# Performance work log

Measured on AMD Instinct MI355X. Metric: run time of the kernel, lower is better.

Reference implementation:

```python
import jax, jax.numpy as jnp
import numpy as np

B, N, C, H = 8, 1024, 768, 12
D = C // H  # head dim
SCALE = D ** -0.5


def setup_inputs() -> dict:
    key = jax.random.key(0)
    ks = jax.random.split(key, 5)
    return {
        "x": jax.random.normal(ks[0], (B, N, C), dtype=jnp.float32),
        "W_qkv": jax.random.normal(ks[1], (C, 3 * C), dtype=jnp.float32) * (C ** -0.5),
        "b_qkv": jax.random.normal(ks[2], (3 * C,), dtype=jnp.float32) * 0.02,
        "W_proj": jax.random.normal(ks[3], (C, C), dtype=jnp.float32) * (C ** -0.5),
        "b_proj": jax.random.normal(ks[4], (C,), dtype=jnp.float32) * 0.02,
    }


def reference(x, W_qkv, b_qkv, W_proj, b_proj):
    b, n, c = x.shape
    qkv = x @ W_qkv + b_qkv                      # [B,N,3C]
    # rearrange 'b n (k h c) -> k b h n c'
    qkv = qkv.reshape(b, n, 3, H, D).transpose(2, 0, 3, 1, 4)
    q, k, v = qkv[0] * SCALE, qkv[1], qkv[2]     # each [B,H,N,D]
    p = jax.nn.softmax(jnp.einsum('bhnd,bhmd->bhnm', q, k), axis=-1)
    o = jnp.einsum('bhnm,bhmd->bhnd', p, v)      # [B,H,N,D]
    o = o.transpose(0, 2, 1, 3).reshape(b, n, c)  # 'b h n c -> b n (h c)'
    return o @ W_proj + b_proj
```

## Files before the change

kernel.cpp:

```cpp
#include <hip/hip_runtime.h>


typedef short  bf16x8_t __attribute__((ext_vector_type(8)));
typedef float  f32x4_t  __attribute__((ext_vector_type(4)));

static __device__ __forceinline__ unsigned short f2bf(float f) {
    union { float f; unsigned u; } v; v.f = f;
    unsigned r = v.u + 0x7fffu + ((v.u >> 16) & 1u);
    return (unsigned short)(r >> 16);
}

typedef __attribute__((address_space(1))) const unsigned gas_u32;
typedef __attribute__((address_space(3))) unsigned las_u32;
static __device__ __forceinline__ void gload16(const void* g, void* l) {
    __builtin_amdgcn_global_load_lds((gas_u32*)g, (las_u32*)l, 16, 0, 0);
}

#define WAIT0 asm volatile("s_waitcnt vmcnt(0)" ::: "memory")
#define BAR   __builtin_amdgcn_s_barrier()

#define STAGE_TILE(DST, SRC, K0, NP, NT)                                   \
    _Pragma("unroll")                                                      \
    for (int p_ = 0; p_ < NP; ++p_) {                                      \
        const int base_ = p_*NT + wb;                                      \
        const int i_ = base_ + lane;                                       \
        const int row_ = i_ >> 3;                                          \
        const int cb_ = ((i_ & 7) ^ (row_ & 7)) * 8;                       \
        gload16((SRC) + (size_t)row_*768 + (K0) + cb_, &(DST)[base_*8]);   \
    }

#define COMPUTE_T(AS, BS)                                                  \
    {                                                                      \
        bf16x8_t a_[2][4], b_[2][4];                                       \
        _Pragma("unroll")                                                  \
        for (int ks_ = 0; ks_ < 2; ++ks_) {                                \
            _Pragma("unroll")                                              \
            for (int m_ = 0; m_ < 4; ++m_) {                               \
                const int ra_ = wm*64 + m_*16 + l15;                       \
                a_[ks_][m_] = *(const bf16x8_t*)&(AS)[ra_*64 + ((ks_*4 + lhi) ^ (ra_ & 7))*8]; \
                const int rb_ = wn*64 + m_*16 + l15;                       \
                b_[ks_][m_] = *(const bf16x8_t*)&(BS)[rb_*64 + ((ks_*4 + lhi) ^ (rb_ & 7))*8]; \
            }                                                              \
        }                                                                  \
        _Pragma("unroll")                                                  \
        for (int m_ = 0; m_ < 4; ++m_)                                     \
            _Pragma("unroll")                                              \
            for (int n_ = 0; n_ < 4; ++n_) {                               \
                acc[m_][n_] = __builtin_amdgcn_mfma_f32_16x16x32_bf16(a_[0][m_], b_[0][n_], acc[m_][n_], 0, 0, 0); \
                acc[m_][n_] = __builtin_amdgcn_mfma_f32_16x16x32_bf16(a_[1][m_], b_[1][n_], acc[m_][n_], 0, 0, 0); \
            }                                                              \
    }

#define COMPUTE_P(AS, BS)                                                  \
    {                                                                      \
        bf16x8_t a_[2][2], b_[2][4];                                       \
        _Pragma("unroll")                                                  \
        for (int ks_ = 0; ks_ < 2; ++ks_) {                                \
            _Pragma("unroll")                                              \
            for (int m_ = 0; m_ < 2; ++m_) {                               \
                const int ra_ = wm*32 + m_*16 + l15;                       \
                a_[ks_][m_] = *(const bf16x8_t*)&(AS)[ra_*64 + ((ks_*4 + lhi) ^ (ra_ & 7))*8]; \
            }                                                              \
            _Pragma("unroll")                                              \
            for (int n_ = 0; n_ < 4; ++n_) {                               \
                const int rb_ = wn*64 + n_*16 + l15;                       \
                b_[ks_][n_] = *(const bf16x8_t*)&(BS)[rb_*64 + ((ks_*4 + lhi) ^ (rb_ & 7))*8]; \
            }                                                              \
        }                                                                  \
        _Pragma("unroll")                                                  \
        for (int m_ = 0; m_ < 2; ++m_)                                     \
            _Pragma("unroll")                                              \
            for (int n_ = 0; n_ < 4; ++n_) {                               \
                acc[m_][n_] = __builtin_amdgcn_mfma_f32_16x16x32_bf16(a_[0][m_], b_[0][n_], acc[m_][n_], 0, 0, 0); \
                acc[m_][n_] = __builtin_amdgcn_mfma_f32_16x16x32_bf16(a_[1][m_], b_[1][n_], acc[m_][n_], 0, 0, 0); \
            }                                                              \
    }

__global__ __launch_bounds__(256) void convert_x(
    const float* __restrict__ src, unsigned short* __restrict__ dst)
{
    const int i = blockIdx.x * 256 + threadIdx.x;
    const float4 v = ((const float4*)src)[i];
    ushort4 o; o.x = f2bf(v.x); o.y = f2bf(v.y); o.z = f2bf(v.z); o.w = f2bf(v.w);
    ((ushort4*)dst)[i] = o;
}

__global__ __launch_bounds__(256) void transpose_cvt(
    const float* __restrict__ src, unsigned short* __restrict__ dst, int R, int C)
{
    __shared__ unsigned short tile[32][33];
    const int tx = threadIdx.x & 31, ty = threadIdx.x >> 5;
    const int bx = blockIdx.x, by = blockIdx.y;
    #pragma unroll
    for (int j = 0; j < 32; j += 8)
        tile[ty + j][tx] = f2bf(src[(size_t)(by*32 + ty + j) * C + bx*32 + tx]);
    __syncthreads();
    #pragma unroll
    for (int j = 0; j < 32; j += 8)
        dst[(size_t)(bx*32 + ty + j) * R + by*32 + tx] = tile[tx][ty + j];
}

__global__ __launch_bounds__(512, 4) void gemm_qkv_bf16(
    const unsigned short* __restrict__ A, const unsigned short* __restrict__ Bt,
    const float* __restrict__ bias,
    unsigned short* __restrict__ q, unsigned short* __restrict__ kO,
    unsigned short* __restrict__ vT)
{
    __shared__ unsigned short As[256*64];
    __shared__ unsigned short Bs[128*64];
    const int tid = threadIdx.x;
    const int id = blockIdx.x;
    const int swz = (id & 7) * 72 + (id >> 3);
    const int n0 = (swz % 18) * 128, m0 = (swz / 18) * 256;

    const int lane = tid & 63, w = tid >> 6;
    const int l15 = lane & 15, lhi = lane >> 4;
    const int wm = w >> 1, wn = w & 1;
    const int wb = tid & 448;

    const unsigned short* Ab = A  + (size_t)m0 * 768;
    const unsigned short* Bb = Bt + (size_t)n0 * 768;

    f32x4_t acc[4][4] = {};

    #pragma unroll 1
    for (int t = 0; t < 12; ++t) {
        STAGE_TILE(As, Ab, t*64, 4, 512)
        STAGE_TILE(Bs, Bb, t*64, 2, 512)
        WAIT0; BAR;
        COMPUTE_T(As, Bs)
        BAR;
    }

    #pragma unroll
    for (int n = 0; n < 4; ++n) {
        const int gcol = n0 + wn*64 + n*16 + l15;
        const int kk = gcol / 768;
        const int r  = gcol - kk*768;
        const int h  = r >> 6, d = r & 63;
        const float bv = bias[gcol];
        const float sc = (kk == 0) ? 0.125f : 1.0f;
        #pragma unroll
        for (int m = 0; m < 4; ++m) {
            const int grow_base = m0 + wm*64 + m*16 + lhi*4;
            #pragma unroll
            for (int reg = 0; reg < 4; ++reg) {
                const int grow = grow_base + reg;
                const int bb = grow >> 10, seq = grow & 1023;
                const unsigned short ov = f2bf((acc[m][n][reg] + bv) * sc);
                const size_t bh = (size_t)bb*12 + h;
                if (kk == 0)      q [ (bh*1024 + seq)*64 + d ] = ov;
                else if (kk == 1) kO[ (bh*1024 + seq)*64 + d ] = ov;
                else              vT[ (bh*64 + d)*1024 + seq ] = ov;
            }
        }
    }
}

__global__ __launch_bounds__(256, 5) void attn2(
    const unsigned short* __restrict__ q, const unsigned short* __restrict__ k,
    const unsigned short* __restrict__ vT, unsigned short* __restrict__ obuf)
{
    __shared__ unsigned short Ks[64 * 72];
    __shared__ unsigned short Vs[64 * 72];
    __shared__ unsigned short P[4][16 * 72];
    const int tid = threadIdx.x;
    const int id = blockIdx.x;
    const int swz = (id & 7) * 192 + (id >> 3);
    const int qt = swz & 15, bh = swz >> 4;

    const int lane = tid & 63, w = tid >> 6;
    const int l15 = lane & 15, lhi = lane >> 4;
    const unsigned short* qp = q  + (size_t)bh * 65536;
    const unsigned short* kp = k  + (size_t)bh * 65536;
    const unsigned short* vp = vT + (size_t)bh * 65536;

    bf16x8_t qf[2];
    const int qrow = qt*64 + w*16 + l15;
    #pragma unroll
    for (int ks = 0; ks < 2; ++ks)
        qf[ks] = *(const bf16x8_t*)(qp + (size_t)qrow*64 + ks*32 + lhi*8);

    f32x4_t acco[4] = {};
    float lsum[4] = {0.f, 0.f, 0.f, 0.f};
    unsigned short* Pw = P[w];

    const int rr = (tid & 127) >> 1 | ((tid >> 7) << 6);
    (void)rr;

    bf16x8_t kr[2], vr[2];
    #pragma unroll
    for (int p = 0; p < 2; ++p) {
        const int idx = p*256 + tid;
        const int r8 = idx >> 3, cb = (idx & 7) * 8;
        kr[p] = *(const bf16x8_t*)(kp + (size_t)r8*64 + cb);
        vr[p] = *(const bf16x8_t*)(vp + (size_t)r8*1024 + cb);
    }
    #pragma unroll
    for (int p = 0; p < 2; ++p) {
        const int idx = p*256 + tid;
        const int r8 = idx >> 3, cb = (idx & 7) * 8;
        *(bf16x8_t*)&Ks[r8*72 + cb] = kr[p];
        *(bf16x8_t*)&Vs[r8*72 + cb] = vr[p];
    }

    for (int kt = 0; kt < 16; ++kt) {
        __syncthreads();
        if (kt < 15) {
            #pragma unroll
            for (int p = 0; p < 2; ++p) {
                const int idx = p*256 + tid;
                const int r8 = idx >> 3, cb = (idx & 7) * 8;
                kr[p] = *(const bf16x8_t*)(kp + (size_t)((kt+1)*64 + r8)*64 + cb);
                vr[p] = *(const bf16x8_t*)(vp + (size_t)r8*1024 + (kt+1)*64 + cb);
            }
        }

        f32x4_t accs[4] = {};
        __builtin_amdgcn_s_setprio(1);
        #pragma unroll
        for (int c = 0; c < 4; ++c)
            #pragma unroll
            for (int ks = 0; ks < 2; ++ks) {
                bf16x8_t kf = *(const bf16x8_t*)&Ks[(c*16 + l15)*72 + ks*32 + lhi*8];
                accs[c] = __builtin_amdgcn_mfma_f32_16x16x32_bf16(qf[ks], kf, accs[c], 0, 0, 0);
            }
        __builtin_amdgcn_s_setprio(0);

        #pragma unroll
        for (int c = 0; c < 4; ++c)
            #pragma unroll
            for (int r = 0; r < 4; ++r) {
                const float pv = __expf(accs[c][r]);
                lsum[r] += pv;
                Pw[(lhi*4 + r)*72 + c*16 + l15] = f2bf(pv);
            }

        bf16x8_t pf[2];
        #pragma unroll
        for (int ks = 0; ks < 2; ++ks)
            pf[ks] = *(const bf16x8_t*)&Pw[l15*72 + ks*32 + lhi*8];
        __builtin_amdgcn_s_setprio(1);
        #pragma unroll
        for (int n = 0; n < 4; ++n)
            #pragma unroll
            for (int ks = 0; ks < 2; ++ks) {
                bf16x8_t vf = *(const bf16x8_t*)&Vs[(n*16 + l15)*72 + ks*32 + lhi*8];
                acco[n] = __builtin_amdgcn_mfma_f32_16x16x32_bf16(pf[ks], vf, acco[n], 0, 0, 0);
            }
        __builtin_amdgcn_s_setprio(0);

        __syncthreads();
        if (kt < 15) {
            #pragma unroll
            for (int p = 0; p < 2; ++p) {
                const int idx = p*256 + tid;
                const int r8 = idx >> 3, cb = (idx & 7) * 8;
                *(bf16x8_t*)&Ks[r8*72 + cb] = kr[p];
                *(bf16x8_t*)&Vs[r8*72 + cb] = vr[p];
            }
        }
    }

    #pragma unroll
    for (int r = 0; r < 4; ++r)
        #pragma unroll
        for (int off = 1; off <= 8; off <<= 1)
            lsum[r] += __shfl_xor(lsum[r], off, 64);

    const int b = bh / 12, h = bh % 12;
    #pragma unroll
    for (int n = 0; n < 4; ++n)
        #pragma unroll
        for (int r = 0; r < 4; ++r) {
            const int seq = qt*64 + w*16 + lhi*4 + r;
            obuf[((size_t)(b*1024 + seq))*768 + h*64 + n*16 + l15] = f2bf(acco[n][r] / lsum[r]);
        }
}

__global__ __launch_bounds__(256, 4) void gemm_proj_bf16(
    const unsigned short* __restrict__ A, const unsigned short* __restrict__ Bt,
    const float* __restrict__ bias, float* __restrict__ out)
{
    __shared__ unsigned short As[64*64];
    __shared__ unsigned short Bs[128*64];
    const int tid = threadIdx.x;
    const int id = blockIdx.x;
    const int swz = (id & 7) * 96 + (id >> 3);
    const int n0 = (swz % 6) * 128, m0 = (swz / 6) * 64;

    const int lane = tid & 63, w = tid >> 6;
    const int l15 = lane & 15, lhi = lane >> 4;
    const int wm = w >> 1, wn = w & 1;
    const int wb = tid & 192;

    const unsigned short* Ab = A  + (size_t)m0 * 768;
    const unsigned short* Bb = Bt + (size_t)n0 * 768;

    f32x4_t acc[2][4] = {};

    #pragma unroll 1
    for (int t = 0; t < 12; ++t) {
        STAGE_TILE(As, Ab, t*64, 2, 256)
        STAGE_TILE(Bs, Bb, t*64, 4, 256)
        WAIT0; BAR;
        COMPUTE_P(As, Bs)
        BAR;
    }

    #pragma unroll
    for (int n = 0; n < 4; ++n) {
        const int gcol = n0 + wn*64 + n*16 + l15;
        const float bv = bias[gcol];
        #pragma unroll
        for (int m = 0; m < 2; ++m) {
            const int grow_base = m0 + wm*32 + m*16 + lhi*4;
            #pragma unroll
            for (int reg = 0; reg < 4; ++reg)
                out[(size_t)(grow_base + reg)*768 + gcol] = acc[m][n][reg] + bv;
        }
    }
}

extern "C" void kernel_launch(void* const* d_in, const int* in_sizes, int n_in,
                              void* d_out, int out_size, void* d_ws, size_t ws_size,
                              hipStream_t stream) {
    const float* x     = (const float*)d_in[0];
    const float* Wqkv  = (const float*)d_in[1];
    const float* bqkv  = (const float*)d_in[2];
    const float* Wproj = (const float*)d_in[3];
    const float* bproj = (const float*)d_in[4];
    float* out = (float*)d_out;
    unsigned short* ws = (unsigned short*)d_ws;

    unsigned short* xb    = ws;
    unsigned short* obuf  = ws;
    unsigned short* wqt   = ws + 6291456u;
    unsigned short* wpt   = ws + 8060928u;
    unsigned short* qb    = ws + 8650752u;
    unsigned short* kb    = ws + 14942208u;
    unsigned short* vTb   = ws + 21233664u;

    convert_x     <<<6144, 256, 0, stream>>>(x, xb);
    transpose_cvt <<<dim3(72, 24), 256, 0, stream>>>(Wqkv, wqt, 768, 2304);
    transpose_cvt <<<dim3(24, 24), 256, 0, stream>>>(Wproj, wpt, 768, 768);
    gemm_qkv_bf16 <<<576, 512, 0, stream>>>(xb, wqt, bqkv, qb, kb, vTb);
    attn2         <<<1536, 256, 0, stream>>>(qb, kb, vTb, obuf);
    gemm_proj_bf16<<<768, 256, 0, stream>>>(obuf, wpt, bproj, out);
}
```

Measured before the change: 136.8 us.

## Restructure QKV GEMM into 256x256 double-buffered tiles with interleaved prefetch

```diff
diff --git a/kernel.cpp b/kernel.cpp
--- a/kernel.cpp
+++ b/kernel.cpp
@@ -18,6 +18,45 @@
 
 #define WAIT0 asm volatile("s_waitcnt vmcnt(0)" ::: "memory")
 #define BAR   __builtin_amdgcn_s_barrier()
+
+#define STAGE_HALF(DST, SRC, K0)                                           \
+    _Pragma("unroll")                                                      \
+    for (int p_ = 0; p_ < 2; ++p_) {                                       \
+        const int base_ = p_*512 + (w << 6);                               \
+        const int i_ = base_ + lane;                                       \
+        const int row_ = i_ >> 3;                                          \
+        const int cb_ = ((i_ & 7) ^ (row_ & 7)) * 8;                       \
+        gload16((SRC) + (size_t)row_*768 + (K0) + cb_, &(DST)[base_*8]);   \
+    }
+
+#define LDA_Q(SLOT, MH)                                                    \
+    _Pragma("unroll")                                                      \
+    for (int ks_ = 0; ks_ < 2; ++ks_)                                      \
+    _Pragma("unroll")                                                      \
+    for (int j_ = 0; j_ < 4; ++j_) {                                       \
+        const int r_ = (MH)*64 + j_*16 + l15;                              \
+        a[ks_][j_] = *(const bf16x8_t*)&(SLOT)[r_*64 + ((ks_*4 + lhi) ^ (l15 & 7))*8]; \
+    }
+
+#define LDB_Q(SLOT, NH)                                                    \
+    _Pragma("unroll")                                                      \
+    for (int ks_ = 0; ks_ < 2; ++ks_)                                      \
+    _Pragma("unroll")                                                      \
+    for (int i_ = 0; i_ < 2; ++i_) {                                       \
+        const int c_ = cb0 + (NH)*32 + i_*16 + l15;                        \
+        b[ks_][i_] = *(const bf16x8_t*)&(SLOT)[c_*64 + ((ks_*4 + lhi) ^ (l15 & 7))*8]; \
+    }
+
+#define MFMA16(MH, NH)                                                     \
+    __builtin_amdgcn_s_setprio(1);                                         \
+    _Pragma("unroll")                                                      \
+    for (int j_ = 0; j_ < 4; ++j_)                                         \
+    _Pragma("unroll")                                                      \
+    for (int i_ = 0; i_ < 2; ++i_) {                                       \
+        acc[(MH)*4 + j_][(NH)*2 + i_] = __builtin_amdgcn_mfma_f32_16x16x32_bf16(a[0][j_], b[0][i_], acc[(MH)*4 + j_][(NH)*2 + i_], 0, 0, 0); \
+        acc[(MH)*4 + j_][(NH)*2 + i_] = __builtin_amdgcn_mfma_f32_16x16x32_bf16(a[1][j_], b[1][i_], acc[(MH)*4 + j_][(NH)*2 + i_], 0, 0, 0); \
+    }                                                                      \
+    __builtin_amdgcn_s_setprio(0);
 
 #define STAGE_TILE(DST, SRC, K0, NP, NT)                                   \
     _Pragma("unroll")                                                      \
@@ -27,28 +66,6 @@
         const int row_ = i_ >> 3;                                          \
         const int cb_ = ((i_ & 7) ^ (row_ & 7)) * 8;                       \
         gload16((SRC) + (size_t)row_*768 + (K0) + cb_, &(DST)[base_*8]);   \
-    }
-
-#define COMPUTE_T(AS, BS)                                                  \
-    {                                                                      \
-        bf16x8_t a_[2][4], b_[2][4];                                       \
-        _Pragma("unroll")                                                  \
-        for (int ks_ = 0; ks_ < 2; ++ks_) {                                \
-            _Pragma("unroll")                                              \
-            for (int m_ = 0; m_ < 4; ++m_) {                               \
-                const int ra_ = wm*64 + m_*16 + l15;                       \
-                a_[ks_][m_] = *(const bf16x8_t*)&(AS)[ra_*64 + ((ks_*4 + lhi) ^ (ra_ & 7))*8]; \
-                const int rb_ = wn*64 + m_*16 + l15;                       \
-                b_[ks_][m_] = *(const bf16x8_t*)&(BS)[rb_*64 + ((ks_*4 + lhi) ^ (rb_ & 7))*8]; \
-            }                                                              \
-        }                                                                  \
-        _Pragma("unroll")                                                  \
-        for (int m_ = 0; m_ < 4; ++m_)                                     \
-            _Pragma("unroll")                                              \
-            for (int n_ = 0; n_ < 4; ++n_) {                               \
-                acc[m_][n_] = __builtin_amdgcn_mfma_f32_16x16x32_bf16(a_[0][m_], b_[0][n_], acc[m_][n_], 0, 0, 0); \
-                acc[m_][n_] = __builtin_amdgcn_mfma_f32_16x16x32_bf16(a_[1][m_], b_[1][n_], acc[m_][n_], 0, 0, 0); \
-            }                                                              \
     }
 
 #define COMPUTE_P(AS, BS)                                                  \
@@ -100,54 +117,104 @@
         dst[(size_t)(bx*32 + ty + j) * R + by*32 + tx] = tile[tx][ty + j];
 }
 
-__global__ __launch_bounds__(512, 4) void gemm_qkv_bf16(
+__global__ __launch_bounds__(512, 2) void gemm_qkv_bf16(
     const unsigned short* __restrict__ A, const unsigned short* __restrict__ Bt,
     const float* __restrict__ bias,
     unsigned short* __restrict__ q, unsigned short* __restrict__ kO,
     unsigned short* __restrict__ vT)
 {
-    __shared__ unsigned short As[256*64];
-    __shared__ unsigned short Bs[128*64];
+    __shared__ unsigned short As[2][2][128*64];
+    __shared__ unsigned short Bs[2][2][128*64];
+
     const int tid = threadIdx.x;
     const int id = blockIdx.x;
-    const int swz = (id & 7) * 72 + (id >> 3);
-    const int n0 = (swz % 18) * 128, m0 = (swz / 18) * 256;
+    const int swz = (id & 7) * 36 + (id >> 3);
+    const int nb = swz % 9, mb = swz / 9;
+    const int n0 = nb * 256, m0 = mb * 256;
 
     const int lane = tid & 63, w = tid >> 6;
     const int l15 = lane & 15, lhi = lane >> 4;
-    const int wm = w >> 1, wn = w & 1;
-    const int wb = tid & 448;
+    const int wm = w >> 2, wn = w & 3;
+    const int cb0 = (wn & 1) * 64;
+    const int bhl = wn >> 1;
 
     const unsigned short* Ab = A  + (size_t)m0 * 768;
     const unsigned short* Bb = Bt + (size_t)n0 * 768;
 
-    f32x4_t acc[4][4] = {};
+    f32x4_t acc[8][4] = {};
+    bf16x8_t a[2][4], b[2][2];
+
+    unsigned short* A0 = As[0][wm];
+    unsigned short* A1 = As[1][wm];
+    unsigned short* B0 = Bs[0][bhl];
+    unsigned short* B1 = Bs[1][bhl];
+
+    STAGE_HALF(As[0][0], Ab,         0)
+    STAGE_HALF(As[0][1], Ab + 98304, 0)
+    STAGE_HALF(Bs[0][0], Bb,         0)
+    STAGE_HALF(Bs[0][1], Bb + 98304, 0)
+    WAIT0; BAR;
 
     #pragma unroll 1
-    for (int t = 0; t < 12; ++t) {
-        STAGE_TILE(As, Ab, t*64, 4, 512)
-        STAGE_TILE(Bs, Bb, t*64, 2, 512)
+    for (int t = 0; t < 6; ++t) {
+        const int k0o = t*128 + 64;
+        const int k0n = t*128 + 128;
+
+        LDA_Q(A0, 0) LDB_Q(B0, 0)
+        STAGE_HALF(As[1][0], Ab,         k0o)
+        STAGE_HALF(As[1][1], Ab + 98304, k0o)
+        BAR; MFMA16(0, 0) BAR;
+
+        LDB_Q(B0, 1)
+        STAGE_HALF(Bs[1][0], Bb,         k0o)
+        STAGE_HALF(Bs[1][1], Bb + 98304, k0o)
+        BAR; MFMA16(0, 1) BAR;
+
+        LDA_Q(A0, 1)
+        BAR; MFMA16(1, 1) BAR;
+
+        LDB_Q(B0, 0)
+        BAR; MFMA16(1, 0)
         WAIT0; BAR;
-        COMPUTE_T(As, Bs)
-        BAR;
-    }
-
-    #pragma unroll
-    for (int n = 0; n < 4; ++n) {
-        const int gcol = n0 + wn*64 + n*16 + l15;
-        const int kk = gcol / 768;
+
+        LDA_Q(A1, 0) LDB_Q(B1, 0)
+        if (t < 5) {
+            STAGE_HALF(As[0][0], Ab,         k0n)
+            STAGE_HALF(As[0][1], Ab + 98304, k0n)
+        }
+        BAR; MFMA16(0, 0) BAR;
+
+        LDB_Q(B1, 1)
+        if (t < 5) {
+            STAGE_HALF(Bs[0][0], Bb,         k0n)
+            STAGE_HALF(Bs[0][1], Bb + 98304, k0n)
+        }
+        BAR; MFMA16(0, 1) BAR;
+
+        LDA_Q(A1, 1)
+        BAR; MFMA16(1, 1) BAR;
+
+        LDB_Q(B1, 0)
+        BAR; MFMA16(1, 0)
+        WAIT0; BAR;
+    }
+
+    const int kk = nb / 3;
+    #pragma unroll
+    for (int nf = 0; nf < 4; ++nf) {
+        const int gcol = n0 + wn*64 + nf*16 + l15;
         const int r  = gcol - kk*768;
         const int h  = r >> 6, d = r & 63;
         const float bv = bias[gcol];
         const float sc = (kk == 0) ? 0.125f : 1.0f;
         #pragma unroll
-        for (int m = 0; m < 4; ++m) {
-            const int grow_base = m0 + wm*64 + m*16 + lhi*4;
+        for (int mf = 0; mf < 8; ++mf) {
+            const int grow_base = m0 + wm*128 + mf*16 + lhi*4;
             #pragma unroll
             for (int reg = 0; reg < 4; ++reg) {
                 const int grow = grow_base + reg;
                 const int bb = grow >> 10, seq = grow & 1023;
-                const unsigned short ov = f2bf((acc[m][n][reg] + bv) * sc);
+                const unsigned short ov = f2bf((acc[mf][nf][reg] + bv) * sc);
                 const size_t bh = (size_t)bb*12 + h;
                 if (kk == 0)      q [ (bh*1024 + seq)*64 + d ] = ov;
                 else if (kk == 1) kO[ (bh*1024 + seq)*64 + d ] = ov;
@@ -185,9 +252,6 @@
     float lsum[4] = {0.f, 0.f, 0.f, 0.f};
     unsigned short* Pw = P[w];
 
-    const int rr = (tid & 127) >> 1 | ((tid >> 7) << 6);
-    (void)rr;
-
     bf16x8_t kr[2], vr[2];
     #pragma unroll
     for (int p = 0; p < 2; ++p) {
@@ -344,7 +408,7 @@
     convert_x     <<<6144, 256, 0, stream>>>(x, xb);
     transpose_cvt <<<dim3(72, 24), 256, 0, stream>>>(Wqkv, wqt, 768, 2304);
     transpose_cvt <<<dim3(24, 24), 256, 0, stream>>>(Wproj, wpt, 768, 768);
-    gemm_qkv_bf16 <<<576, 512, 0, stream>>>(xb, wqt, bqkv, qb, kb, vTb);
+    gemm_qkv_bf16 <<<288, 512, 0, stream>>>(xb, wqt, bqkv, qb, kb, vTb);
     attn2         <<<1536, 256, 0, stream>>>(qb, kb, vTb, obuf);
     gemm_proj_bf16<<<768, 256, 0, stream>>>(obuf, wpt, bproj, out);
 }
```

Result: slower. 162.3 us (+18.7%).

## Replace LDS-staged QKV GEMM with direct global-to-register loads and smaller tiles

Applied to the files above, without the earlier changes.

```diff
diff --git a/kernel.cpp b/kernel.cpp
--- a/kernel.cpp
+++ b/kernel.cpp
@@ -27,28 +27,6 @@
         const int row_ = i_ >> 3;                                          \
         const int cb_ = ((i_ & 7) ^ (row_ & 7)) * 8;                       \
         gload16((SRC) + (size_t)row_*768 + (K0) + cb_, &(DST)[base_*8]);   \
-    }
-
-#define COMPUTE_T(AS, BS)                                                  \
-    {                                                                      \
-        bf16x8_t a_[2][4], b_[2][4];                                       \
-        _Pragma("unroll")                                                  \
-        for (int ks_ = 0; ks_ < 2; ++ks_) {                                \
-            _Pragma("unroll")                                              \
-            for (int m_ = 0; m_ < 4; ++m_) {                               \
-                const int ra_ = wm*64 + m_*16 + l15;                       \
-                a_[ks_][m_] = *(const bf16x8_t*)&(AS)[ra_*64 + ((ks_*4 + lhi) ^ (ra_ & 7))*8]; \
-                const int rb_ = wn*64 + m_*16 + l15;                       \
-                b_[ks_][m_] = *(const bf16x8_t*)&(BS)[rb_*64 + ((ks_*4 + lhi) ^ (rb_ & 7))*8]; \
-            }                                                              \
-        }                                                                  \
-        _Pragma("unroll")                                                  \
-        for (int m_ = 0; m_ < 4; ++m_)                                     \
-            _Pragma("unroll")                                              \
-            for (int n_ = 0; n_ < 4; ++n_) {                               \
-                acc[m_][n_] = __builtin_amdgcn_mfma_f32_16x16x32_bf16(a_[0][m_], b_[0][n_], acc[m_][n_], 0, 0, 0); \
-                acc[m_][n_] = __builtin_amdgcn_mfma_f32_16x16x32_bf16(a_[1][m_], b_[1][n_], acc[m_][n_], 0, 0, 0); \
-            }                                                              \
     }
 
 #define COMPUTE_P(AS, BS)                                                  \
@@ -100,36 +78,46 @@
         dst[(size_t)(bx*32 + ty + j) * R + by*32 + tx] = tile[tx][ty + j];
 }
 
-__global__ __launch_bounds__(512, 4) void gemm_qkv_bf16(
+__global__ __launch_bounds__(256, 3) void gemm_qkv_bf16(
     const unsigned short* __restrict__ A, const unsigned short* __restrict__ Bt,
     const float* __restrict__ bias,
     unsigned short* __restrict__ q, unsigned short* __restrict__ kO,
     unsigned short* __restrict__ vT)
 {
-    __shared__ unsigned short As[256*64];
-    __shared__ unsigned short Bs[128*64];
     const int tid = threadIdx.x;
     const int id = blockIdx.x;
-    const int swz = (id & 7) * 72 + (id >> 3);
-    const int n0 = (swz % 18) * 128, m0 = (swz / 18) * 256;
+    const int swz = (id & 7) * 144 + (id >> 3);
+    const int n0 = (swz % 18) * 128, m0 = (swz / 18) * 128;
 
     const int lane = tid & 63, w = tid >> 6;
     const int l15 = lane & 15, lhi = lane >> 4;
     const int wm = w >> 1, wn = w & 1;
-    const int wb = tid & 448;
-
-    const unsigned short* Ab = A  + (size_t)m0 * 768;
-    const unsigned short* Bb = Bt + (size_t)n0 * 768;
+
+    const unsigned short* Aw = A  + (size_t)(m0 + wm*64) * 768;
+    const unsigned short* Bw = Bt + (size_t)(n0 + wn*64) * 768;
 
     f32x4_t acc[4][4] = {};
 
     #pragma unroll 1
     for (int t = 0; t < 12; ++t) {
-        STAGE_TILE(As, Ab, t*64, 4, 512)
-        STAGE_TILE(Bs, Bb, t*64, 2, 512)
-        WAIT0; BAR;
-        COMPUTE_T(As, Bs)
-        BAR;
+        const int K0 = t * 64;
+        bf16x8_t a[2][4], b[2][4];
+        #pragma unroll
+        for (int ks = 0; ks < 2; ++ks) {
+            #pragma unroll
+            for (int m = 0; m < 4; ++m)
+                a[ks][m] = *(const bf16x8_t*)(Aw + (size_t)(m*16 + l15)*768 + K0 + ks*32 + lhi*8);
+            #pragma unroll
+            for (int n = 0; n < 4; ++n)
+                b[ks][n] = *(const bf16x8_t*)(Bw + (size_t)(n*16 + l15)*768 + K0 + ks*32 + lhi*8);
+        }
+        #pragma unroll
+        for (int m = 0; m < 4; ++m)
+            #pragma unroll
+            for (int n = 0; n < 4; ++n) {
+                acc[m][n] = __builtin_amdgcn_mfma_f32_16x16x32_bf16(a[0][m], b[0][n], acc[m][n], 0, 0, 0);
+                acc[m][n] = __builtin_amdgcn_mfma_f32_16x16x32_bf16(a[1][m], b[1][n], acc[m][n], 0, 0, 0);
+            }
     }
 
     #pragma unroll
@@ -184,9 +172,6 @@
     f32x4_t acco[4] = {};
     float lsum[4] = {0.f, 0.f, 0.f, 0.f};
     unsigned short* Pw = P[w];
-
-    const int rr = (tid & 127) >> 1 | ((tid >> 7) << 6);
-    (void)rr;
 
     bf16x8_t kr[2], vr[2];
     #pragma unroll
@@ -344,7 +329,7 @@
     convert_x     <<<6144, 256, 0, stream>>>(x, xb);
     transpose_cvt <<<dim3(72, 24), 256, 0, stream>>>(Wqkv, wqt, 768, 2304);
     transpose_cvt <<<dim3(24, 24), 256, 0, stream>>>(Wproj, wpt, 768, 768);
-    gemm_qkv_bf16 <<<576, 512, 0, stream>>>(xb, wqt, bqkv, qb, kb, vTb);
+    gemm_qkv_bf16 <<<1152, 256, 0, stream>>>(xb, wqt, bqkv, qb, kb, vTb);
     attn2         <<<1536, 256, 0, stream>>>(qb, kb, vTb, obuf);
     gemm_proj_bf16<<<768, 256, 0, stream>>>(obuf, wpt, bproj, out);
 }
```

Measured after the change: 228.0 us. 66.7% more time.

## Double-buffer QKV GEMM LDS tiles and shrink block tile to 128x128

Applied to the files above, without the earlier changes.

```diff
diff --git a/kernel.cpp b/kernel.cpp
--- a/kernel.cpp
+++ b/kernel.cpp
@@ -16,8 +16,67 @@
     __builtin_amdgcn_global_load_lds((gas_u32*)g, (las_u32*)l, 16, 0, 0);
 }
 
+#define WAIT8 asm volatile("s_waitcnt vmcnt(8)" ::: "memory")
 #define WAIT0 asm volatile("s_waitcnt vmcnt(0)" ::: "memory")
 #define BAR   __builtin_amdgcn_s_barrier()
+
+#define STAGE_T(DST, SRC, K0)                                              \
+    _Pragma("unroll")                                                      \
+    for (int p_ = 0; p_ < 4; ++p_) {                                       \
+        const int base_ = p_*256 + w64;                                    \
+        const int i_ = base_ + lane;                                       \
+        const int row_ = i_ >> 3;                                          \
+        const int cb_ = ((i_ & 7) ^ (row_ & 7)) * 8;                       \
+        gload16((SRC) + (size_t)row_*768 + (K0) + cb_, &(DST)[base_*8]);   \
+    }
+
+#define COMPUTE_T(AS, BS)                                                  \
+    {                                                                      \
+        bf16x8_t a_[2][4], b_[2][4];                                       \
+        _Pragma("unroll")                                                  \
+        for (int ks_ = 0; ks_ < 2; ++ks_) {                                \
+            _Pragma("unroll")                                              \
+            for (int m_ = 0; m_ < 4; ++m_) {                               \
+                const int ra_ = wm*64 + m_*16 + l15;                       \
+                a_[ks_][m_] = *(const bf16x8_t*)&(AS)[ra_*64 + ((ks_*4 + lhi) ^ (ra_ & 7))*8]; \
+                const int rb_ = wn*64 + m_*16 + l15;                       \
+                b_[ks_][m_] = *(const bf16x8_t*)&(BS)[rb_*64 + ((ks_*4 + lhi) ^ (rb_ & 7))*8]; \
+            }                                                              \
+        }                                                                  \
+        _Pragma("unroll")                                                  \
+        for (int m_ = 0; m_ < 4; ++m_)                                     \
+            _Pragma("unroll")                                              \
+            for (int n_ = 0; n_ < 4; ++n_) {                               \
+                acc[m_][n_] = __builtin_amdgcn_mfma_f32_16x16x32_bf16(a_[0][m_], b_[0][n_], acc[m_][n_], 0, 0, 0); \
+                acc[m_][n_] = __builtin_amdgcn_mfma_f32_16x16x32_bf16(a_[1][m_], b_[1][n_], acc[m_][n_], 0, 0, 0); \
+            }                                                              \
+    }
+
+#define GEMM_MAIN_LOOP(Ab, Bb)                                             \
+    STAGE_T(As0, Ab, 0)                                                    \
+    STAGE_T(Bs0, Bb, 0)                                                    \
+    STAGE_T(As1, Ab, 64)                                                   \
+    STAGE_T(Bs1, Bb, 64)                                                   \
+    _Pragma("unroll 1")                                                    \
+    for (int t = 0; t < 6; ++t) {                                          \
+        WAIT8; BAR;                                                        \
+        COMPUTE_T(As0, Bs0)                                                \
+        BAR;                                                               \
+        if (t < 5) {                                                       \
+            STAGE_T(As0, Ab, t*128 + 128)                                  \
+            STAGE_T(Bs0, Bb, t*128 + 128)                                  \
+            WAIT8;                                                         \
+        } else {                                                           \
+            WAIT0;                                                         \
+        }                                                                  \
+        BAR;                                                               \
+        COMPUTE_T(As1, Bs1)                                                \
+        BAR;                                                               \
+        if (t < 5) {                                                       \
+            STAGE_T(As1, Ab, t*128 + 192)                                  \
+            STAGE_T(Bs1, Bb, t*128 + 192)                                  \
+        }                                                                  \
+    }
 
 #define STAGE_TILE(DST, SRC, K0, NP, NT)                                   \
     _Pragma("unroll")                                                      \
@@ -29,28 +88,6 @@
         gload16((SRC) + (size_t)row_*768 + (K0) + cb_, &(DST)[base_*8]);   \
     }
 
-#define COMPUTE_T(AS, BS)                                                  \
-    {                                                                      \
-        bf16x8_t a_[2][4], b_[2][4];                                       \
-        _Pragma("unroll")                                                  \
-        for (int ks_ = 0; ks_ < 2; ++ks_) {                                \
-            _Pragma("unroll")                                              \
-            for (int m_ = 0; m_ < 4; ++m_) {                               \
-                const int ra_ = wm*64 + m_*16 + l15;                       \
-                a_[ks_][m_] = *(const bf16x8_t*)&(AS)[ra_*64 + ((ks_*4 + lhi) ^ (ra_ & 7))*8]; \
-                const int rb_ = wn*64 + m_*16 + l15;                       \
-                b_[ks_][m_] = *(const bf16x8_t*)&(BS)[rb_*64 + ((ks_*4 + lhi) ^ (rb_ & 7))*8]; \
-            }                                                              \
-        }                                                                  \
-        _Pragma("unroll")                                                  \
-        for (int m_ = 0; m_ < 4; ++m_)                                     \
-            _Pragma("unroll")                                              \
-            for (int n_ = 0; n_ < 4; ++n_) {                               \
-                acc[m_][n_] = __builtin_amdgcn_mfma_f32_16x16x32_bf16(a_[0][m_], b_[0][n_], acc[m_][n_], 0, 0, 0); \
-                acc[m_][n_] = __builtin_amdgcn_mfma_f32_16x16x32_bf16(a_[1][m_], b_[1][n_], acc[m_][n_], 0, 0, 0); \
-            }                                                              \
-    }
-
 #define COMPUTE_P(AS, BS)                                                  \
     {                                                                      \
         bf16x8_t a_[2][2], b_[2][4];                                       \
@@ -100,37 +137,30 @@
         dst[(size_t)(bx*32 + ty + j) * R + by*32 + tx] = tile[tx][ty + j];
 }
 
-__global__ __launch_bounds__(512, 4) void gemm_qkv_bf16(
+__global__ __launch_bounds__(256) void gemm_qkv_bf16(
     const unsigned short* __restrict__ A, const unsigned short* __restrict__ Bt,
     const float* __restrict__ bias,
     unsigned short* __restrict__ q, unsigned short* __restrict__ kO,
     unsigned short* __restrict__ vT)
 {
-    __shared__ unsigned short As[256*64];
-    __shared__ unsigned short Bs[128*64];
+    __shared__ unsigned short As0[128*64], As1[128*64];
+    __shared__ unsigned short Bs0[128*64], Bs1[128*64];
     const int tid = threadIdx.x;
     const int id = blockIdx.x;
-    const int swz = (id & 7) * 72 + (id >> 3);
-    const int n0 = (swz % 18) * 128, m0 = (swz / 18) * 256;
+    const int swz = (id & 7) * 144 + (id >> 3);
+    const int n0 = (swz % 18) * 128, m0 = (swz / 18) * 128;
 
     const int lane = tid & 63, w = tid >> 6;
     const int l15 = lane & 15, lhi = lane >> 4;
     const int wm = w >> 1, wn = w & 1;
-    const int wb = tid & 448;
+    const int w64 = tid & 192;
 
     const unsigned short* Ab = A  + (size_t)m0 * 768;
     const unsigned short* Bb = Bt + (size_t)n0 * 768;
 
     f32x4_t acc[4][4] = {};
 
-    #pragma unroll 1
-    for (int t = 0; t < 12; ++t) {
-        STAGE_TILE(As, Ab, t*64, 4, 512)
-        STAGE_TILE(Bs, Bb, t*64, 2, 512)
-        WAIT0; BAR;
-        COMPUTE_T(As, Bs)
-        BAR;
-    }
+    GEMM_MAIN_LOOP(Ab, Bb)
 
     #pragma unroll
     for (int n = 0; n < 4; ++n) {
@@ -184,9 +214,6 @@
     f32x4_t acco[4] = {};
     float lsum[4] = {0.f, 0.f, 0.f, 0.f};
     unsigned short* Pw = P[w];
-
-    const int rr = (tid & 127) >> 1 | ((tid >> 7) << 6);
-    (void)rr;
 
     bf16x8_t kr[2], vr[2];
     #pragma unroll
@@ -344,7 +371,7 @@
     convert_x     <<<6144, 256, 0, stream>>>(x, xb);
     transpose_cvt <<<dim3(72, 24), 256, 0, stream>>>(Wqkv, wqt, 768, 2304);
     transpose_cvt <<<dim3(24, 24), 256, 0, stream>>>(Wproj, wpt, 768, 768);
-    gemm_qkv_bf16 <<<576, 512, 0, stream>>>(xb, wqt, bqkv, qb, kb, vTb);
+    gemm_qkv_bf16 <<<1152, 256, 0, stream>>>(xb, wqt, bqkv, qb, kb, vTb);
     attn2         <<<1536, 256, 0, stream>>>(qb, kb, vTb, obuf);
     gemm_proj_bf16<<<768, 256, 0, stream>>>(obuf, wpt, bproj, out);
 }
```

After: 140.3 us. 2.6% more time.
